# Kernel optimization log

Hardware: AMD Instinct MI355X
Metric: run time of the kernel (lower is better)

The kernel has to match this reference:

```python
import jax, jax.numpy as jnp
import numpy as np

# tiny-cuda-nn HashGrid config from the module
N_LEVELS = 12
F_PER_LEVEL = 2
LOG2_T = 16
T = 1 << LOG2_T            # 65536 entries per level
BASE_RES = 4
PER_LEVEL_SCALE = 1.61
HASH_PRIME_Y = np.uint32(2654435761)
HIDDEN = 256
OUT = 3
N_POINTS = 1048576

# per-level scale / resolution (tcnn: scale = base*s^l - 1, res = ceil(scale)+1)
_LEVEL_SCALES = [BASE_RES * (PER_LEVEL_SCALE ** l) - 1.0 for l in range(N_LEVELS)]
_LEVEL_RES = [int(np.ceil(s)) + 1 for s in _LEVEL_SCALES]

_CORNERS = np.array([[0, 0], [1, 0], [0, 1], [1, 1]], dtype=np.uint32)  # [4,2]


def hash_encode(x, tables):
    """x: [N,2] in [0,1); tables: [L,T,F]. Returns [N, L*F]."""
    offs_u = jnp.asarray(_CORNERS)                      # [4,2] uint32
    offs_f = offs_u.astype(x.dtype)                     # [4,2]
    feats = []
    for l in range(N_LEVELS):
        s = _LEVEL_SCALES[l]
        res = _LEVEL_RES[l]
        pos = x * jnp.asarray(s, x.dtype) + 0.5         # [N,2]
        p0f = jnp.floor(pos)
        w = pos - p0f                                   # [N,2] frac, differentiable
        p0 = p0f.astype(jnp.uint32)                     # [N,2]
        c = p0[:, None, :] + offs_u[None]               # [N,4,2] corner coords
        # bilinear weight per corner: prod over dims of (w if offset==1 else 1-w)
        wc = jnp.where(offs_f[None] == 1.0, w[:, None, :], 1.0 - w[:, None, :]).prod(-1)  # [N,4]
        if res * res <= T:
            # dense (tight grid) indexing
            cx = jnp.minimum(c[..., 0], np.uint32(res - 1))
            cy = jnp.minimum(c[..., 1], np.uint32(res - 1))
            idx = cx + cy * np.uint32(res)
        else:
            # spatial hash: x*1 XOR y*prime, masked to table size
            idx = (c[..., 0] ^ (c[..., 1] * HASH_PRIME_Y)) & np.uint32(T - 1)
        f = tables[l][idx.astype(jnp.int32)]            # [N,4,F] gather
        feats.append((wc[..., None] * f).sum(axis=1))   # [N,F]
    return jnp.concatenate(feats, axis=-1)              # [N, L*F]


def setup_inputs() -> dict:
    key = jax.random.key(0)
    ks = jax.random.split(key, 10)
    x = jax.random.uniform(ks[0], (N_POINTS, 2), dtype=jnp.float32)
    # tcnn initializes hash tables uniform in [-1e-4, 1e-4]
    tables = jax.random.uniform(ks[1], (N_LEVELS, T, F_PER_LEVEL), dtype=jnp.float32,
                                minval=-1e-4, maxval=1e-4)
    d_in = N_LEVELS * F_PER_LEVEL

    def lin(k, fan_in, fan_out):
        bound = 1.0 / np.sqrt(fan_in)
        kw, kb = jax.random.split(k)
        W = jax.random.uniform(kw, (fan_in, fan_out), dtype=jnp.float32, minval=-bound, maxval=bound)
        b = jax.random.uniform(kb, (fan_out,), dtype=jnp.float32, minval=-bound, maxval=bound)
        return W, b

    W1, b1 = lin(ks[2], d_in, HIDDEN)
    W2, b2 = lin(ks[3], HIDDEN, HIDDEN)
    W3, b3 = lin(ks[4], HIDDEN, HIDDEN)
    Wo, bo = lin(ks[5], HIDDEN, OUT)
    return {"x": x, "tables": tables, "W1": W1, "b1": b1, "W2": W2, "b2": b2,
            "W3": W3, "b3": b3, "Wo": Wo, "bo": bo}


def reference(x, tables, W1, b1, W2, b2, W3, b3, Wo, bo):
    enc = hash_encode(x, tables)                        # [N,24]
    h = jax.nn.relu(enc @ W1 + b1)
    h = jax.nn.relu(h @ W2 + b2)
    h = jax.nn.relu(h @ W3 + b3)
    return h @ Wo + bo                                  # [N,3]
```

## Files before the change

### kernel.cpp

```cpp
#include <hip/hip_runtime.h>

typedef _Float16 f16;
typedef _Float16 f16x2 __attribute__((ext_vector_type(2)));
typedef _Float16 f16x4 __attribute__((ext_vector_type(4)));
typedef _Float16 f16x8 __attribute__((ext_vector_type(8)));
typedef float    f32x4 __attribute__((ext_vector_type(4)));

#define ES 40
#define NPTS 128

static __device__ const float c_scale[12] = {
  3.0f, 5.44f, 9.3684f, 15.693124f, 25.87592964f, 42.2702467204f,
  68.665097219844f, 111.16080652394884f, 179.5788985035576f,
  289.7320265907278f, 467.0785628110717f, 752.6064861258255f };
static __device__ const unsigned c_res[12] = {4,7,11,17,27,44,70,113,181,291,469,754};

__global__ __launch_bounds__(256) void prep_weights(
    const float* __restrict__ W1, const float* __restrict__ W2,
    const float* __restrict__ W3, const float* __restrict__ Wo,
    f16* __restrict__ ws)
{
  int i = blockIdx.x * 256 + threadIdx.x;
  if (i < 8192) {
    int o = i >> 5, k = i & 31;
    ws[i] = (k < 24) ? (f16)W1[k * 256 + o] : (f16)0.0f;
  } else if (i < 73728) {
    int j = i - 8192; int o = j >> 8, k = j & 255;
    ws[i] = (f16)W2[k * 256 + o];
  } else if (i < 139264) {
    int j = i - 73728; int o = j >> 8, k = j & 255;
    ws[i] = (f16)W3[k * 256 + o];
  } else if (i < 143360) {
    int j = i - 139264; int o = j >> 8, k = j & 255;
    ws[i] = (o < 3) ? (f16)Wo[k * 3 + o] : (f16)0.0f;
  }
}

__device__ __forceinline__ f16x2 enc_level_dense(
    float2 xy, float s, unsigned res, const float* __restrict__ tbl)
{
  float px = __fadd_rn(__fmul_rn(xy.x, s), 0.5f);
  float py = __fadd_rn(__fmul_rn(xy.y, s), 0.5f);
  float fx = floorf(px), fy = floorf(py);
  float wx = px - fx, wy = py - fy;
  unsigned ix = (unsigned)fx, iy = (unsigned)fy;
  unsigned rm = res - 1u;
  unsigned x0 = min(ix, rm);
  unsigned y0 = min(iy, rm), y1 = min(iy + 1u, rm);
  bool xe = (ix >= rm);
  f32x4 r0 = *(const f32x4*)(tbl + (x0 + y0 * res) * 2);
  f32x4 r1 = *(const f32x4*)(tbl + (x0 + y1 * res) * 2);
  float f00x = r0[0], f00y = r0[1];
  float f10x = xe ? r0[0] : r0[2], f10y = xe ? r0[1] : r0[3];
  float f01x = r1[0], f01y = r1[1];
  float f11x = xe ? r1[0] : r1[2], f11y = xe ? r1[1] : r1[3];
  float w00 = (1.f - wx) * (1.f - wy), w10 = wx * (1.f - wy);
  float w01 = (1.f - wx) * wy,         w11 = wx * wy;
  float e0 = w00 * f00x + w10 * f10x + w01 * f01x + w11 * f11x;
  float e1 = w00 * f00y + w10 * f10y + w01 * f01y + w11 * f11y;
  f16x2 pk; pk[0] = (f16)e0; pk[1] = (f16)e1;
  return pk;
}

__device__ __forceinline__ f16x2 enc_level_hash(
    float2 xy, float s, const float* __restrict__ tbl)
{
  float px = __fadd_rn(__fmul_rn(xy.x, s), 0.5f);
  float py = __fadd_rn(__fmul_rn(xy.y, s), 0.5f);
  float fx = floorf(px), fy = floorf(py);
  float wx = px - fx, wy = py - fy;
  unsigned ix = (unsigned)fx, iy = (unsigned)fy;
  unsigned h0 = iy * 2654435761u, h1 = (iy + 1u) * 2654435761u;
  unsigned i00 = (ix ^ h0) & 65535u,  i10 = ((ix + 1u) ^ h0) & 65535u;
  unsigned i01 = (ix ^ h1) & 65535u,  i11 = ((ix + 1u) ^ h1) & 65535u;
  const float2* tb = (const float2*)tbl;
  float2 f00 = tb[i00], f10 = tb[i10], f01 = tb[i01], f11 = tb[i11];
  float w00 = (1.f - wx) * (1.f - wy), w10 = wx * (1.f - wy);
  float w01 = (1.f - wx) * wy,         w11 = wx * wy;
  float e0 = w00 * f00.x + w10 * f10.x + w01 * f01.x + w11 * f11.x;
  float e1 = w00 * f00.y + w10 * f10.y + w01 * f01.y + w11 * f11.y;
  f16x2 pk; pk[0] = (f16)e0; pk[1] = (f16)e1;
  return pk;
}

template<bool NEXT_OUT>
__device__ __forceinline__ void layer256_pipe(
    f16* __restrict__ h, const f16* __restrict__ WT,
    const f32x4* bv, f16x8* cur0, f16x8* cur1,
    const f16* __restrict__ WTn, const float* __restrict__ bn,
    f16x8* nxt0, f16x8* nxt1, f32x4* bvn, f16x8* aout,
    const int* vbase, const int* wbase, int w, int l15, int g)
{
  f32x4 acc[4][8];
  #pragma unroll
  for (int mt = 0; mt < 4; ++mt)
    #pragma unroll
    for (int nt = 0; nt < 8; ++nt) acc[mt][nt] = bv[mt];

  f16x8 abuf[3][4];
  #pragma unroll
  for (int mt = 0; mt < 4; ++mt) { abuf[0][mt] = cur0[mt]; abuf[1][mt] = cur1[mt]; }

  const char* hb = (const char*)h;
  #pragma unroll
  for (int ks = 0; ks < 8; ++ks) {
    if (ks < 6) {
      #pragma unroll
      for (int mt = 0; mt < 4; ++mt)
        abuf[(ks+2)%3][mt] = *(const f16x8*)(WT + (w*64 + mt*16 + l15)*256 + (ks+2)*32 + g*8);
    } else if (ks == 6) {
      if (NEXT_OUT) {
        #pragma unroll
        for (int q = 0; q < 4; ++q)
          aout[q] = *(const f16x8*)(WTn + l15*256 + q*32 + g*8);
      } else {
        #pragma unroll
        for (int mt = 0; mt < 4; ++mt)
          nxt0[mt] = *(const f16x8*)(WTn + (w*64 + mt*16 + l15)*256 + g*8);
        #pragma unroll
        for (int mt = 0; mt < 4; ++mt)
          bvn[mt] = *(const f32x4*)(bn + w*64 + mt*16 + g*4);
      }
    } else {
      if (NEXT_OUT) {
        #pragma unroll
        for (int q = 0; q < 4; ++q)
          aout[4+q] = *(const f16x8*)(WTn + l15*256 + (4+q)*32 + g*8);
      } else {
        #pragma unroll
        for (int mt = 0; mt < 4; ++mt)
          nxt1[mt] = *(const f16x8*)(WTn + (w*64 + mt*16 + l15)*256 + 32 + g*8);
      }
    }
    #pragma unroll
    for (int nt = 0; nt < 8; ++nt) {
      f16x8 b = *(const f16x8*)(hb + vbase[ks] + nt*8192);
      #pragma unroll
      for (int mt = 0; mt < 4; ++mt)
        acc[mt][nt] = __builtin_amdgcn_mfma_f32_16x16x32_f16(abuf[ks%3][mt], b, acc[mt][nt], 0, 0, 0);
    }
  }
  __syncthreads();
  #pragma unroll
  for (int mt = 0; mt < 4; ++mt) {
    #pragma unroll
    for (int nt = 0; nt < 8; ++nt) {
      f16x4 hv;
      #pragma unroll
      for (int r = 0; r < 4; ++r)
        hv[r] = (f16)fmaxf(acc[mt][nt][r], 0.0f);
      *(f16x4*)((char*)h + wbase[mt] + nt*8192) = hv;
    }
  }
  __syncthreads();
}

__global__ __launch_bounds__(256, 2) void hashmlp_kernel(
    const float* __restrict__ x, const float* __restrict__ tables,
    const float* __restrict__ b1, const float* __restrict__ b2,
    const float* __restrict__ b3, const float* __restrict__ bo,
    const f16* __restrict__ ws, float* __restrict__ out)
{
  __shared__ __align__(16) f16 s_enc[NPTS * ES];
  __shared__ __align__(16) f16 s_h[NPTS * 256];

  const int tid = threadIdx.x;
  const int blk = blockIdx.x;
  const int w = tid >> 6, lane = tid & 63;
  const int l15 = lane & 15, g = lane >> 4;

  const f16* W1T = ws;
  const f16* W2T = ws + 8192;
  const f16* W3T = ws + 73728;
  const f16* WoT = ws + 139264;

  f16x8 a1[4], pn0[4], pn1[4];
  f32x4 bvA[4], bvB[4];
  #pragma unroll
  for (int mt = 0; mt < 4; ++mt) {
    a1[mt]  = *(const f16x8*)(W1T + (w*64 + mt*16 + l15)*32 + g*8);
    pn0[mt] = *(const f16x8*)(W2T + (w*64 + mt*16 + l15)*256 + g*8);
    pn1[mt] = *(const f16x8*)(W2T + (w*64 + mt*16 + l15)*256 + 32 + g*8);
    bvA[mt] = *(const f32x4*)(b1 + w*64 + mt*16 + g*4);
    bvB[mt] = *(const f32x4*)(b2 + w*64 + mt*16 + g*4);
  }
  float bo0 = bo[0], bo1 = bo[1], bo2 = bo[2];

  int vbase[8], wbase[4];
  {
    int K = (l15 & 7) << 4;
    #pragma unroll
    for (int ks = 0; ks < 8; ++ks)
      vbase[ks] = l15*512 + ((ks*64 + g*16) ^ K);
    #pragma unroll
    for (int mt = 0; mt < 4; ++mt)
      wbase[mt] = l15*512 + (((w*64 + mt*16 + g*4)*2) ^ K);
  }

  {
    int p = tid >> 1, sub = tid & 1;
    int gp = blk * NPTS + p;
    float2 xy = ((const float2*)x)[gp];
    #pragma unroll
    for (int j = 0; j < 5; ++j) {
      int l = j * 2 + sub;
      f16x2 pk = enc_level_dense(xy, c_scale[l], c_res[l], tables + l * 131072);
      *(f16x2*)(&s_enc[p * ES + l * 2]) = pk;
    }
    {
      int l = 10 + sub;
      f16x2 pk = enc_level_hash(xy, c_scale[l], tables + l * 131072);
      *(f16x2*)(&s_enc[p * ES + l * 2]) = pk;
    }
    f16x4 z; z[0] = (f16)0.0f; z[1] = (f16)0.0f; z[2] = (f16)0.0f; z[3] = (f16)0.0f;
    *(f16x4*)(&s_enc[p * ES + 24 + sub * 4]) = z;
  }
  __syncthreads();

  {
    f32x4 acc[4][8];
    #pragma unroll
    for (int mt = 0; mt < 4; ++mt)
      #pragma unroll
      for (int nt = 0; nt < 8; ++nt) acc[mt][nt] = bvA[mt];
    #pragma unroll
    for (int nt = 0; nt < 8; ++nt) {
      f16x8 b = *(const f16x8*)(&s_enc[(nt*16 + l15) * ES + g*8]);
      #pragma unroll
      for (int mt = 0; mt < 4; ++mt)
        acc[mt][nt] = __builtin_amdgcn_mfma_f32_16x16x32_f16(a1[mt], b, acc[mt][nt], 0, 0, 0);
    }
    #pragma unroll
    for (int mt = 0; mt < 4; ++mt) {
      #pragma unroll
      for (int nt = 0; nt < 8; ++nt) {
        f16x4 hv;
        #pragma unroll
        for (int r = 0; r < 4; ++r)
          hv[r] = (f16)fmaxf(acc[mt][nt][r], 0.0f);
        *(f16x4*)((char*)s_h + wbase[mt] + nt*8192) = hv;
      }
    }
  }
  __syncthreads();

  f16x8 qn0[4], qn1[4], aout[8];
  f32x4 bvC[4];
  layer256_pipe<false>(s_h, W2T, bvB, pn0, pn1, W3T, b3, qn0, qn1, bvC, aout,
                       vbase, wbase, w, l15, g);
  layer256_pipe<true >(s_h, W3T, bvC, qn0, qn1, WoT, nullptr, pn0, pn1, bvC, aout,
                       vbase, wbase, w, l15, g);

  {
    f32x4 acc0 = (f32x4)0.0f, acc1 = (f32x4)0.0f;
    const char* hb = (const char*)s_h;
    #pragma unroll
    for (int ks = 0; ks < 8; ++ks) {
      f16x8 b0 = *(const f16x8*)(hb + vbase[ks] + (2*w+0)*8192);
      f16x8 b1v = *(const f16x8*)(hb + vbase[ks] + (2*w+1)*8192);
      acc0 = __builtin_amdgcn_mfma_f32_16x16x32_f16(aout[ks], b0, acc0, 0, 0, 0);
      acc1 = __builtin_amdgcn_mfma_f32_16x16x32_f16(aout[ks], b1v, acc1, 0, 0, 0);
    }
    if (g == 0) {
      int gp0 = blk * NPTS + (2*w+0) * 16 + l15;
      int gp1 = blk * NPTS + (2*w+1) * 16 + l15;
      out[gp0 * 3 + 0] = acc0[0] + bo0;
      out[gp0 * 3 + 1] = acc0[1] + bo1;
      out[gp0 * 3 + 2] = acc0[2] + bo2;
      out[gp1 * 3 + 0] = acc1[0] + bo0;
      out[gp1 * 3 + 1] = acc1[1] + bo1;
      out[gp1 * 3 + 2] = acc1[2] + bo2;
    }
  }
}

extern "C" void kernel_launch(void* const* d_in, const int* in_sizes, int n_in,
                              void* d_out, int out_size, void* d_ws, size_t ws_size,
                              hipStream_t stream) {
  const float* x  = (const float*)d_in[0];
  const float* tb = (const float*)d_in[1];
  const float* W1 = (const float*)d_in[2];
  const float* b1 = (const float*)d_in[3];
  const float* W2 = (const float*)d_in[4];
  const float* b2 = (const float*)d_in[5];
  const float* W3 = (const float*)d_in[6];
  const float* b3 = (const float*)d_in[7];
  const float* Wo = (const float*)d_in[8];
  const float* bo = (const float*)d_in[9];
  f16* ws = (f16*)d_ws;

  prep_weights<<<560, 256, 0, stream>>>(W1, W2, W3, Wo, ws);
  hashmlp_kernel<<<8192, 256, 0, stream>>>(x, tb, b1, b2, b3, bo, ws, (float*)d_out);
}
```

Measured before the change: 353.7 us.

## Switch hidden layers to 32x32x16 MFMA with 2x2 wave tiling

The hidden-layer GEMMs move from 16x16x32 MFMA tiles, where each wave covered 64 outputs by all 128 points, to 32x32x16 MFMA with a 2x2 wave grid in which each wave covers 128 outputs by 64 points. The goal is to cut LDS reads of activations per MFMA and to use the larger, more efficient MFMA shape. The cross-layer prefetch of weights into registers is removed, so weights are now loaded from global memory or cache inside the k loop without software pipelining. This may expose load latency in exchange for a simpler schedule and less register pressure.

```diff
diff --git a/kernel.cpp b/kernel.cpp
--- a/kernel.cpp
+++ b/kernel.cpp
@@ -4,7 +4,8 @@
 typedef _Float16 f16x2 __attribute__((ext_vector_type(2)));
 typedef _Float16 f16x4 __attribute__((ext_vector_type(4)));
 typedef _Float16 f16x8 __attribute__((ext_vector_type(8)));
-typedef float    f32x4 __attribute__((ext_vector_type(4)));
+typedef float    f32x4  __attribute__((ext_vector_type(4)));
+typedef float    f32x16 __attribute__((ext_vector_type(16)));
 
 #define ES 40
 #define NPTS 128
@@ -83,75 +84,53 @@
   return pk;
 }
 
-template<bool NEXT_OUT>
-__device__ __forceinline__ void layer256_pipe(
-    f16* __restrict__ h, const f16* __restrict__ WT,
-    const f32x4* bv, f16x8* cur0, f16x8* cur1,
-    const f16* __restrict__ WTn, const float* __restrict__ bn,
-    f16x8* nxt0, f16x8* nxt1, f32x4* bvn, f16x8* aout,
-    const int* vbase, const int* wbase, int w, int l15, int g)
-{
-  f32x4 acc[4][8];
+__device__ __forceinline__ void layer256_32(
+    f16* __restrict__ h, const f16* __restrict__ WT, const float* __restrict__ bias,
+    int wm, const int* bb, int KX, int l31, int g2)
+{
+  f32x16 acc[4][2];
+  #pragma unroll
+  for (int mt = 0; mt < 4; ++mt) {
+    #pragma unroll
+    for (int rq = 0; rq < 4; ++rq) {
+      f32x4 t = *(const f32x4*)(bias + wm*128 + mt*32 + rq*8 + g2*4);
+      #pragma unroll
+      for (int j = 0; j < 4; ++j) {
+        acc[mt][0][rq*4+j] = t[j];
+        acc[mt][1][rq*4+j] = t[j];
+      }
+    }
+  }
+  const char* hb = (const char*)h;
+  #pragma unroll
+  for (int ks = 0; ks < 16; ++ks) {
+    f16x8 a[4], b[2];
+    #pragma unroll
+    for (int mt = 0; mt < 4; ++mt)
+      a[mt] = *(const f16x8*)(WT + (wm*128 + mt*32 + l31)*256 + ks*16 + g2*8);
+    int off = (ks*32 + g2*16) ^ KX;
+    b[0] = *(const f16x8*)(hb + bb[0] + off);
+    b[1] = *(const f16x8*)(hb + bb[1] + off);
+    #pragma unroll
+    for (int mt = 0; mt < 4; ++mt) {
+      acc[mt][0] = __builtin_amdgcn_mfma_f32_32x32x16_f16(a[mt], b[0], acc[mt][0], 0, 0, 0);
+      acc[mt][1] = __builtin_amdgcn_mfma_f32_32x32x16_f16(a[mt], b[1], acc[mt][1], 0, 0, 0);
+    }
+  }
+  __syncthreads();
   #pragma unroll
   for (int mt = 0; mt < 4; ++mt)
     #pragma unroll
-    for (int nt = 0; nt < 8; ++nt) acc[mt][nt] = bv[mt];
-
-  f16x8 abuf[3][4];
-  #pragma unroll
-  for (int mt = 0; mt < 4; ++mt) { abuf[0][mt] = cur0[mt]; abuf[1][mt] = cur1[mt]; }
-
-  const char* hb = (const char*)h;
-  #pragma unroll
-  for (int ks = 0; ks < 8; ++ks) {
-    if (ks < 6) {
-      #pragma unroll
-      for (int mt = 0; mt < 4; ++mt)
-        abuf[(ks+2)%3][mt] = *(const f16x8*)(WT + (w*64 + mt*16 + l15)*256 + (ks+2)*32 + g*8);
-    } else if (ks == 6) {
-      if (NEXT_OUT) {
+    for (int nt = 0; nt < 2; ++nt)
+      #pragma unroll
+      for (int rq = 0; rq < 4; ++rq) {
+        f16x4 hv;
         #pragma unroll
-        for (int q = 0; q < 4; ++q)
-          aout[q] = *(const f16x8*)(WTn + l15*256 + q*32 + g*8);
-      } else {
-        #pragma unroll
-        for (int mt = 0; mt < 4; ++mt)
-          nxt0[mt] = *(const f16x8*)(WTn + (w*64 + mt*16 + l15)*256 + g*8);
-        #pragma unroll
-        for (int mt = 0; mt < 4; ++mt)
-          bvn[mt] = *(const f32x4*)(bn + w*64 + mt*16 + g*4);
-      }
-    } else {
-      if (NEXT_OUT) {
-        #pragma unroll
-        for (int q = 0; q < 4; ++q)
-          aout[4+q] = *(const f16x8*)(WTn + l15*256 + (4+q)*32 + g*8);
-      } else {
-        #pragma unroll
-        for (int mt = 0; mt < 4; ++mt)
-          nxt1[mt] = *(const f16x8*)(WTn + (w*64 + mt*16 + l15)*256 + 32 + g*8);
-      }
-    }
-    #pragma unroll
-    for (int nt = 0; nt < 8; ++nt) {
-      f16x8 b = *(const f16x8*)(hb + vbase[ks] + nt*8192);
-      #pragma unroll
-      for (int mt = 0; mt < 4; ++mt)
-        acc[mt][nt] = __builtin_amdgcn_mfma_f32_16x16x32_f16(abuf[ks%3][mt], b, acc[mt][nt], 0, 0, 0);
-    }
-  }
-  __syncthreads();
-  #pragma unroll
-  for (int mt = 0; mt < 4; ++mt) {
-    #pragma unroll
-    for (int nt = 0; nt < 8; ++nt) {
-      f16x4 hv;
-      #pragma unroll
-      for (int r = 0; r < 4; ++r)
-        hv[r] = (f16)fmaxf(acc[mt][nt][r], 0.0f);
-      *(f16x4*)((char*)h + wbase[mt] + nt*8192) = hv;
-    }
-  }
+        for (int j = 0; j < 4; ++j)
+          hv[j] = (f16)fmaxf(acc[mt][nt][rq*4+j], 0.0f);
+        int ob = (wm*128 + mt*32 + rq*8 + g2*4) * 2;
+        *(f16x4*)((char*)h + bb[nt] + (ob ^ KX)) = hv;
+      }
   __syncthreads();
 }
 
@@ -167,35 +146,19 @@
   const int tid = threadIdx.x;
   const int blk = blockIdx.x;
   const int w = tid >> 6, lane = tid & 63;
-  const int l15 = lane & 15, g = lane >> 4;
+  const int wm = w >> 1, wn = w & 1;
+  const int l31 = lane & 31, g2 = lane >> 5;
+  const int l15 = lane & 15, g4 = lane >> 4;
 
   const f16* W1T = ws;
   const f16* W2T = ws + 8192;
   const f16* W3T = ws + 73728;
   const f16* WoT = ws + 139264;
 
-  f16x8 a1[4], pn0[4], pn1[4];
-  f32x4 bvA[4], bvB[4];
-  #pragma unroll
-  for (int mt = 0; mt < 4; ++mt) {
-    a1[mt]  = *(const f16x8*)(W1T + (w*64 + mt*16 + l15)*32 + g*8);
-    pn0[mt] = *(const f16x8*)(W2T + (w*64 + mt*16 + l15)*256 + g*8);
-    pn1[mt] = *(const f16x8*)(W2T + (w*64 + mt*16 + l15)*256 + 32 + g*8);
-    bvA[mt] = *(const f32x4*)(b1 + w*64 + mt*16 + g*4);
-    bvB[mt] = *(const f32x4*)(b2 + w*64 + mt*16 + g*4);
-  }
-  float bo0 = bo[0], bo1 = bo[1], bo2 = bo[2];
-
-  int vbase[8], wbase[4];
-  {
-    int K = (l15 & 7) << 4;
-    #pragma unroll
-    for (int ks = 0; ks < 8; ++ks)
-      vbase[ks] = l15*512 + ((ks*64 + g*16) ^ K);
-    #pragma unroll
-    for (int mt = 0; mt < 4; ++mt)
-      wbase[mt] = l15*512 + (((w*64 + mt*16 + g*4)*2) ^ K);
-  }
+  const int KX = (l31 & 7) << 4;
+  int bb[2];
+  bb[0] = (wn*64 +  0 + l31) * 512;
+  bb[1] = (wn*64 + 32 + l31) * 512;
 
   {
     int p = tid >> 1, sub = tid & 1;
@@ -218,50 +181,71 @@
   __syncthreads();
 
   {
-    f32x4 acc[4][8];
+    f32x16 acc[4][2];
+    #pragma unroll
+    for (int mt = 0; mt < 4; ++mt) {
+      #pragma unroll
+      for (int rq = 0; rq < 4; ++rq) {
+        f32x4 t = *(const f32x4*)(b1 + wm*128 + mt*32 + rq*8 + g2*4);
+        #pragma unroll
+        for (int j = 0; j < 4; ++j) {
+          acc[mt][0][rq*4+j] = t[j];
+          acc[mt][1][rq*4+j] = t[j];
+        }
+      }
+    }
+    const char* eb = (const char*)s_enc;
+    #pragma unroll
+    for (int ks = 0; ks < 2; ++ks) {
+      f16x8 a[4], b[2];
+      #pragma unroll
+      for (int mt = 0; mt < 4; ++mt)
+        a[mt] = *(const f16x8*)(W1T + (wm*128 + mt*32 + l31)*32 + ks*16 + g2*8);
+      b[0] = *(const f16x8*)(eb + (wn*64 +  0 + l31)*80 + ks*32 + g2*16);
+      b[1] = *(const f16x8*)(eb + (wn*64 + 32 + l31)*80 + ks*32 + g2*16);
+      #pragma unroll
+      for (int mt = 0; mt < 4; ++mt) {
+        acc[mt][0] = __builtin_amdgcn_mfma_f32_32x32x16_f16(a[mt], b[0], acc[mt][0], 0, 0, 0);
+        acc[mt][1] = __builtin_amdgcn_mfma_f32_32x32x16_f16(a[mt], b[1], acc[mt][1], 0, 0, 0);
+      }
+    }
     #pragma unroll
     for (int mt = 0; mt < 4; ++mt)
       #pragma unroll
-      for (int nt = 0; nt < 8; ++nt) acc[mt][nt] = bvA[mt];
-    #pragma unroll
-    for (int nt = 0; nt < 8; ++nt) {
-      f16x8 b = *(const f16x8*)(&s_enc[(nt*16 + l15) * ES + g*8]);
-      #pragma unroll
-      for (int mt = 0; mt < 4; ++mt)
-        acc[mt][nt] = __builtin_amdgcn_mfma_f32_16x16x32_f16(a1[mt], b, acc[mt][nt], 0, 0, 0);
-    }
-    #pragma unroll
-    for (int mt = 0; mt < 4; ++mt) {
-      #pragma unroll
-      for (int nt = 0; nt < 8; ++nt) {
-        f16x4 hv;
+      for (int nt = 0; nt < 2; ++nt)
         #pragma unroll
-        for (int r = 0; r < 4; ++r)
-          hv[r] = (f16)fmaxf(acc[mt][nt][r], 0.0f);
-        *(f16x4*)((char*)s_h + wbase[mt] + nt*8192) = hv;
-      }
-    }
-  }
-  __syncthreads();
-
-  f16x8 qn0[4], qn1[4], aout[8];
-  f32x4 bvC[4];
-  layer256_pipe<false>(s_h, W2T, bvB, pn0, pn1, W3T, b3, qn0, qn1, bvC, aout,
-                       vbase, wbase, w, l15, g);
-  layer256_pipe<true >(s_h, W3T, bvC, qn0, qn1, WoT, nullptr, pn0, pn1, bvC, aout,
-                       vbase, wbase, w, l15, g);
+        for (int rq = 0; rq < 4; ++rq) {
+          f16x4 hv;
+          #pragma unroll
+          for (int j = 0; j < 4; ++j)
+            hv[j] = (f16)fmaxf(acc[mt][nt][rq*4+j], 0.0f);
+          int ob = (wm*128 + mt*32 + rq*8 + g2*4) * 2;
+          *(f16x4*)((char*)s_h + bb[nt] + (ob ^ KX)) = hv;
+        }
+  }
+  __syncthreads();
+
+  layer256_32(s_h, W2T, b2, wm, bb, KX, l31, g2);
+  layer256_32(s_h, W3T, b3, wm, bb, KX, l31, g2);
 
   {
+    f16x8 aout[8];
+    #pragma unroll
+    for (int ks = 0; ks < 8; ++ks)
+      aout[ks] = *(const f16x8*)(WoT + l15*256 + ks*32 + g4*8);
+    const int KO = (l15 & 7) << 4;
     f32x4 acc0 = (f32x4)0.0f, acc1 = (f32x4)0.0f;
     const char* hb = (const char*)s_h;
     #pragma unroll
     for (int ks = 0; ks < 8; ++ks) {
-      f16x8 b0 = *(const f16x8*)(hb + vbase[ks] + (2*w+0)*8192);
-      f16x8 b1v = *(const f16x8*)(hb + vbase[ks] + (2*w+1)*8192);
+      int off = (ks*64 + g4*16) ^ KO;
+      f16x8 b0 = *(const f16x8*)(hb + (2*w+0)*8192 + l15*512 + off);
+      f16x8 b1v = *(const f16x8*)(hb + (2*w+1)*8192 + l15*512 + off);
       acc0 = __builtin_amdgcn_mfma_f32_16x16x32_f16(aout[ks], b0, acc0, 0, 0, 0);
       acc1 = __builtin_amdgcn_mfma_f32_16x16x32_f16(aout[ks], b1v, acc1, 0, 0, 0);
     }
-    if (g == 0) {
+    if (g4 == 0) {
+      float bo0 = bo[0], bo1 = bo[1], bo2 = bo[2];
       int gp0 = blk * NPTS + (2*w+0) * 16 + l15;
       int gp1 = blk * NPTS + (2*w+1) * 16 + l15;
       out[gp0 * 3 + 0] = acc0[0] + bo0;
```

After: 599.0 us. 1.69x slower.
